# Performance work log

Hardware: AMD Instinct MI355X
Metric: run time of the kernel (lower is better)

The kernel has to match this reference:

```python
import jax, jax.numpy as jnp
import numpy as np

TEMPERATURE = 0.1
B, S, D, V = 4, 256, 768, 50257


def setup_inputs() -> dict:
    key = jax.random.key(0)
    k1, k2 = jax.random.split(key)
    return {
        "pred_embeds": jax.random.normal(k1, (B, S, D), dtype=jnp.float32),
        "embed_weight": jax.random.normal(k2, (V, D), dtype=jnp.float32),
    }


def reference(pred_embeds, embed_weight):
    # metric == 'l2': scores = -||p - t||^2, computed via the GEMM identity
    # -(||p||^2 + ||t||^2 - 2 p.t) instead of a (B,S,V,D) broadcast diff.
    p_sq = jnp.sum(pred_embeds * pred_embeds, axis=-1)        # (B,S)
    t_sq = jnp.sum(embed_weight * embed_weight, axis=-1)      # (V,)
    dot = jnp.einsum('bsd,vd->bsv', pred_embeds, embed_weight)  # (B,S,V)
    scores = 2.0 * dot - p_sq[..., None] - t_sq               # (B,S,V)

    softmax_pred_probs = jax.nn.softmax(scores / TEMPERATURE, axis=-1)
    predictions = jnp.argmax(softmax_pred_probs, axis=-1)      # (B,S) int

    # straight-through one-hot over probs
    y_hard = jax.nn.one_hot(predictions, V, dtype=softmax_pred_probs.dtype)
    pred_probs = y_hard - jax.lax.stop_gradient(softmax_pred_probs) + softmax_pred_probs

    # straight-through embedding lookup
    n_pred_embs = embed_weight[predictions]                    # (B,S,D)
    pred_embeds_st = pred_embeds + jax.lax.stop_gradient(n_pred_embs - pred_embeds)

    return (pred_embeds_st, pred_embeds, predictions, pred_probs, softmax_pred_probs)
```

## Files before the change

kernel.cpp:

```cpp
#include <hip/hip_runtime.h>
#include <math.h>

namespace {

constexpr int Bb = 4, Ss = 256, Dd = 768, Vv = 50257;
constexpr int Mm = Bb * Ss;
constexpr int BM = 128, BN = 128, BK = 32;
constexpr int NS = Dd / BK;
constexpr int TW = (Vv + BN - 1) / BN;
constexpr int TA = Mm / BM;
constexpr int NT2 = TW * 2;
constexpr int CHUNK = BM * BK;
constexpr float SC = 14.4269504088896341f;

constexpr int PSTRIDE = 17;
constexpr int PCOUNT  = 128 * 2 * PSTRIDE;
constexpr size_t SMEM_BYTES = (size_t)PCOUNT * 4 * 3;

typedef _Float16 f16x8 __attribute__((ext_vector_type(8)));
typedef float f32x4 __attribute__((ext_vector_type(4)));

constexpr size_t WPLANE = (size_t)TW * NS * CHUNK;
constexpr size_t APLANE = (size_t)TA * NS * CHUNK;

__device__ __forceinline__ void gload_lds16(const void* g, void* l) {
    typedef __attribute__((address_space(3))) void lds_t;
    typedef const __attribute__((address_space(1))) void gm_t;
    __builtin_amdgcn_global_load_lds((gm_t*)g, (lds_t*)l, 16, 0, 0);
}

__global__ __launch_bounds__(256) void convert_pack_tsq(const float* __restrict__ srcW,
                                                        const float* __restrict__ srcA,
                                                        _Float16* __restrict__ Whp,
                                                        _Float16* __restrict__ Wlp,
                                                        _Float16* __restrict__ Ahp,
                                                        _Float16* __restrict__ Alp,
                                                        float* __restrict__ tsq,
                                                        float* __restrict__ asq) {
    const bool isW = blockIdx.x < TW;
    const int t    = isW ? blockIdx.x : (blockIdx.x - TW);
    const int nrows = isW ? Vv : Mm;
    const float* __restrict__ src = isW ? srcW : srcA;
    _Float16* __restrict__ hp = isW ? Whp : Ahp;
    _Float16* __restrict__ lp = isW ? Wlp : Alp;
    float* __restrict__ sumsq = isW ? tsq : asq;

    const int tid = threadIdx.x;
    const int r   = blockIdx.y * 64 + (tid >> 2);
    const int q   = tid & 3;
    const int v   = t * BM + r;
    const bool valid = v < nrows;

    float sq = 0.f;
#pragma unroll
    for (int i = 0; i < 6; ++i) {
        const int s = q * 6 + i;
        float vals[32];
        if (valid) {
            const float4* p = reinterpret_cast<const float4*>(src + (size_t)v * Dd + s * BK);
#pragma unroll
            for (int k = 0; k < 8; ++k) *reinterpret_cast<float4*>(&vals[4 * k]) = p[k];
        } else {
#pragma unroll
            for (int k = 0; k < 32; ++k) vals[k] = 0.f;
        }
        const size_t chunk = ((size_t)t * NS + s) * CHUNK;
#pragma unroll
        for (int fq = 0; fq < 4; ++fq) {
            _Float16 hi8[8], lo8[8];
#pragma unroll
            for (int e = 0; e < 8; ++e) {
                const float x = vals[fq * 8 + e];
                sq = fmaf(x, x, sq);
                const _Float16 h = (_Float16)x;
                hi8[e] = h;
                lo8[e] = (_Float16)(x - (float)h);
            }
            *reinterpret_cast<f16x8*>(&hp[chunk + fq * (BM * 8) + (size_t)r * 8]) =
                *reinterpret_cast<const f16x8*>(hi8);
            *reinterpret_cast<f16x8*>(&lp[chunk + fq * (BM * 8) + (size_t)r * 8]) =
                *reinterpret_cast<const f16x8*>(lo8);
        }
    }
    sq += __shfl_xor(sq, 1);
    sq += __shfl_xor(sq, 2);
    if (valid && q == 0) sumsq[v] = sq;
}

__global__ __launch_bounds__(256) void gemm_kernel(const _Float16* __restrict__ Ahp,
                                                   const _Float16* __restrict__ Alp,
                                                   const _Float16* __restrict__ Whp,
                                                   const _Float16* __restrict__ Wlp,
                                                   const float* __restrict__ tsq,
                                                   float* __restrict__ scores,
                                                   float* __restrict__ pmax,
                                                   int*   __restrict__ pidx,
                                                   float* __restrict__ psum) {
    __shared__ __align__(16) char smem_raw[SMEM_BYTES];
    _Float16 (*lds)[CHUNK] = reinterpret_cast<_Float16(*)[CHUNK]>(smem_raw);

    const int b    = blockIdx.x;
    const int xcd  = b & 7;
    const int slot = b >> 3;
    const int tn   = xcd * 50 + (slot >> 3);
    const int tm   = slot & 7;
    if (tn >= TW) return;

    const int tid  = threadIdx.x;
    const int wid  = tid >> 6;
    const int lane = tid & 63;
    const int wr   = wid >> 1;
    const int wc   = wid & 1;
    const int fr   = lane & 15;
    const int fq   = lane >> 4;

    const _Float16* gA_h = Ahp + (size_t)tm * NS * CHUNK;
    const _Float16* gA_l = Alp + (size_t)tm * NS * CHUNK;
    const _Float16* gW_h = Whp + (size_t)tn * NS * CHUNK;
    const _Float16* gW_l = Wlp + (size_t)tn * NS * CHUNK;

    f32x4 acc[4][4];
#pragma unroll
    for (int m = 0; m < 4; ++m)
#pragma unroll
        for (int n = 0; n < 4; ++n) acc[m][n] = (f32x4){0.f, 0.f, 0.f, 0.f};

    for (int s = 0; s < NS; ++s) {
        if (s) __syncthreads();
        const size_t so = (size_t)s * CHUNK;
        const _Float16* gsrc[4] = {gA_h + so, gA_l + so, gW_h + so, gW_l + so};
#pragma unroll
        for (int c = 0; c < 4; ++c) {
#pragma unroll
            for (int i = 0; i < 2; ++i) {
                const int seg = wid * 2 + i;
                gload_lds16(gsrc[c] + seg * 512 + lane * 8, &lds[c][seg * 512]);
            }
        }
        __syncthreads();

        f16x8 ah[4], al[4];
#pragma unroll
        for (int m = 0; m < 4; ++m) {
            const int r = wr * 64 + m * 16 + fr;
            ah[m] = *reinterpret_cast<const f16x8*>(&lds[0][fq * (BM * 8) + r * 8]);
            al[m] = *reinterpret_cast<const f16x8*>(&lds[1][fq * (BM * 8) + r * 8]);
        }
#pragma unroll
        for (int n = 0; n < 4; ++n) {
            const int c = wc * 64 + n * 16 + fr;
            const f16x8 wh = *reinterpret_cast<const f16x8*>(&lds[2][fq * (BM * 8) + c * 8]);
            const f16x8 wl = *reinterpret_cast<const f16x8*>(&lds[3][fq * (BM * 8) + c * 8]);
#pragma unroll
            for (int m = 0; m < 4; ++m) {
                acc[m][n] = __builtin_amdgcn_mfma_f32_16x16x32_f16(ah[m], wh, acc[m][n], 0, 0, 0);
                acc[m][n] = __builtin_amdgcn_mfma_f32_16x16x32_f16(al[m], wh, acc[m][n], 0, 0, 0);
                acc[m][n] = __builtin_amdgcn_mfma_f32_16x16x32_f16(ah[m], wl, acc[m][n], 0, 0, 0);
            }
        }
    }

    __syncthreads();
    float* pmL = reinterpret_cast<float*>(smem_raw);
    float* psL = pmL + PCOUNT;
    int*   piL = reinterpret_cast<int*>(psL + PCOUNT);

    float tq[4];
    int   gcol[4];
    bool  ok[4];
#pragma unroll
    for (int n = 0; n < 4; ++n) {
        gcol[n] = tn * BN + wc * 64 + n * 16 + fr;
        ok[n]   = gcol[n] < Vv;
        tq[n]   = ok[n] ? tsq[gcol[n]] : 0.f;
    }

#pragma unroll
    for (int m = 0; m < 4; ++m) {
#pragma unroll
        for (int r = 0; r < 4; ++r) {
            const int rloc = wr * 64 + m * 16 + fq * 4 + r;
            const int grow = tm * BM + rloc;
            float vmax = -INFINITY;
            int   vidx = 0x7fffffff;
#pragma unroll
            for (int n = 0; n < 4; ++n) {
                if (ok[n]) {
                    const float sv = fmaf(2.f, acc[m][n][r], -tq[n]);
                    scores[(size_t)grow * Vv + gcol[n]] = sv;
                    if (sv > vmax) { vmax = sv; vidx = gcol[n]; }
                }
            }
            float ls = 0.f;
#pragma unroll
            for (int n = 0; n < 4; ++n) {
                if (ok[n]) {
                    const float sv = fmaf(2.f, acc[m][n][r], -tq[n]);
                    ls += exp2f((sv - vmax) * SC);
                }
            }
            const int o = (rloc * 2 + wc) * PSTRIDE + fr;
            pmL[o] = vmax;
            psL[o] = ls;
            piL[o] = vidx;
        }
    }
    __syncthreads();

    {
        const int rloc = tid >> 1;
        const int wcs  = tid & 1;
        float m = -INFINITY, s = 0.f;
        int   id = 0x7fffffff;
#pragma unroll
        for (int f = 0; f < 16; ++f) {
            const int o = (rloc * 2 + wcs) * PSTRIDE + f;
            const float m2 = pmL[o];
            const int   i2 = piL[o];
            const float s2 = psL[o];
            if (m2 > m || (m2 == m && i2 < id)) {
                s = ((m > -INFINITY) ? s * exp2f((m - m2) * SC) : 0.f) + s2;
                m = m2; id = i2;
            } else {
                s += s2 * exp2f((m2 - m) * SC);
            }
        }
        const int grow = tm * BM + rloc;
        const int cidx = tn * 2 + wcs;
        const size_t o = (size_t)grow * NT2 + cidx;
        pmax[o] = m;
        pidx[o] = id;
        psum[o] = s;
    }
}

__global__ __launch_bounds__(256) void reduce_stats(const float* __restrict__ pmax,
                                                    const int*   __restrict__ pidx,
                                                    const float* __restrict__ psum,
                                                    float* __restrict__ out1,
                                                    float* __restrict__ out2) {
    const int row = blockIdx.x;
    const int tid = threadIdx.x;
    const size_t base = (size_t)row * NT2;

    float m = -INFINITY, s = 0.f;
    int   id = 0x7fffffff;
    for (int c = tid; c < NT2; c += 256) {
        const float m2 = pmax[base + c];
        const int   i2 = pidx[base + c];
        const float s2 = psum[base + c];
        if (m2 > m || (m2 == m && i2 < id)) {
            s = ((m > -INFINITY) ? s * exp2f((m - m2) * SC) : 0.f) + s2;
            m = m2; id = i2;
        } else {
            s += (m2 > -INFINITY) ? s2 * exp2f((m2 - m) * SC) : 0.f;
        }
    }

    __shared__ float smax[256];
    __shared__ int   sidx[256];
    __shared__ float ssum[256];
    smax[tid] = m; sidx[tid] = id; ssum[tid] = s;
    __syncthreads();
#pragma unroll
    for (int off = 128; off > 0; off >>= 1) {
        if (tid < off) {
            const float m1 = smax[tid], m2 = smax[tid + off];
            const int   i1 = sidx[tid], i2 = sidx[tid + off];
            const float s1 = ssum[tid], s2 = ssum[tid + off];
            if (m2 > m1 || (m2 == m1 && i2 < i1)) {
                smax[tid] = m2; sidx[tid] = i2;
                ssum[tid] = ((m1 > -INFINITY) ? s1 * exp2f((m1 - m2) * SC) : 0.f) + s2;
            } else {
                ssum[tid] = s1 + ((m2 > -INFINITY) ? s2 * exp2f((m2 - m1) * SC) : 0.f);
            }
        }
        __syncthreads();
    }
    if (tid == 0) {
        out2[row] = (float)sidx[0];
        out1[(size_t)row * Dd + 766] = smax[0];
        out1[(size_t)row * Dd + 767] = 1.0f / ssum[0];
    }
}

__global__ __launch_bounds__(256) void finalize_kernel(const float* __restrict__ A,
                                                       const float* __restrict__ W,
                                                       float* __restrict__ out0,
                                                       float* __restrict__ out1,
                                                       float* __restrict__ out2,
                                                       float* __restrict__ out3,
                                                       float* __restrict__ out4) {
    const int row = blockIdx.x;
    const int tid = threadIdx.x;
    float* srow = out4 + (size_t)row * Vv;
    float* hrow = out3 + (size_t)row * Vv;
    constexpr int NV4 = Vv >> 2;

    const float gmax = out1[(size_t)row * Dd + 766];
    const float inv  = out1[(size_t)row * Dd + 767];
    const int   pred = (int)out2[row];

    const float4* s4 = reinterpret_cast<const float4*>(srow);
    float4* p4 = reinterpret_cast<float4*>(srow);
    float4* h4 = reinterpret_cast<float4*>(hrow);
    for (int i = tid; i < NV4; i += 256) {
        const float4 v = s4[i];
        const int b = 4 * i;
        float4 p, h;
        p.x = exp2f((v.x - gmax) * SC) * inv;
        p.y = exp2f((v.y - gmax) * SC) * inv;
        p.z = exp2f((v.z - gmax) * SC) * inv;
        p.w = exp2f((v.w - gmax) * SC) * inv;
        h.x = (b + 0 == pred) ? 1.f : 0.f;
        h.y = (b + 1 == pred) ? 1.f : 0.f;
        h.z = (b + 2 == pred) ? 1.f : 0.f;
        h.w = (b + 3 == pred) ? 1.f : 0.f;
        p4[i] = p;
        h4[i] = h;
    }
    if (tid == 0) {
        const float val = srow[Vv - 1];
        srow[Vv - 1] = exp2f((val - gmax) * SC) * inv;
        hrow[Vv - 1] = (pred == Vv - 1) ? 1.f : 0.f;
    }

    __syncthreads();

    const float4* wrow = reinterpret_cast<const float4*>(W + (size_t)pred * Dd);
    const float4* arow = reinterpret_cast<const float4*>(A + (size_t)row * Dd);
    float4* o0 = reinterpret_cast<float4*>(out0 + (size_t)row * Dd);
    float4* o1 = reinterpret_cast<float4*>(out1 + (size_t)row * Dd);
    if (tid < Dd / 4) {
        o0[tid] = wrow[tid];
        o1[tid] = arow[tid];
    }
}

}

extern "C" void kernel_launch(void* const* d_in, const int* in_sizes, int n_in,
                              void* d_out, int out_size, void* d_ws, size_t ws_size,
                              hipStream_t stream) {
    const float* pred_embeds  = (const float*)d_in[0];
    const float* embed_weight = (const float*)d_in[1];

    float* out  = (float*)d_out;
    float* out0 = out;
    float* out1 = out0 + (size_t)Mm * Dd;
    float* out2 = out1 + (size_t)Mm * Dd;
    float* out3 = out2 + Mm;
    float* out4 = out3 + (size_t)Mm * Vv;

    _Float16* Whp = (_Float16*)out3;
    _Float16* Wlp = Whp + WPLANE;
    _Float16* Ahp = Wlp + WPLANE;
    _Float16* Alp = Ahp + APLANE;
    float*    tsq = (float*)(Alp + APLANE);
    float*    asq = tsq + Vv;
    float*    pmax = asq + Mm;
    int*      pidx = (int*)(pmax + (size_t)Mm * NT2);
    float*    psum = (float*)(pidx + (size_t)Mm * NT2);

    convert_pack_tsq<<<dim3(TW + TA, 2), 256, 0, stream>>>(embed_weight, pred_embeds,
                                                           Whp, Wlp, Ahp, Alp, tsq, asq);

    gemm_kernel<<<3200, 256, 0, stream>>>(Ahp, Alp, Whp, Wlp, tsq, out4,
                                          pmax, pidx, psum);

    reduce_stats<<<Mm, 256, 0, stream>>>(pmax, pidx, psum, out1, out2);

    finalize_kernel<<<Mm, 256, 0, stream>>>(pred_embeds, embed_weight,
                                            out0, out1, out2, out3, out4);
}
```

Measured before the change: 490.0 us.

## Widen GEMM tile to 128x256 with 512 threads and fold reduce into finalize

The GEMM tile grows from 128x128 to 128x256 and runs with 8 waves per 512-thread block, so each A tile is reused across twice as many vocab columns. The tile-to-XCD mapping and the packed W layout are rebuilt to match. Row stats are now merged across lanes with shuffles inside the epilogue, and the separate reduce_stats kernel is removed, with its merge moved to the start of finalize_kernel. This cuts redundant A loads, one kernel launch and the epilogue LDS traffic, at the cost of more waves per block and fewer blocks, which may hurt occupancy or tail balance.

After: 654.0 us. 33.5% more time.

```diff
diff --git a/kernel.cpp b/kernel.cpp
--- a/kernel.cpp
+++ b/kernel.cpp
@@ -5,23 +5,24 @@
 
 constexpr int Bb = 4, Ss = 256, Dd = 768, Vv = 50257;
 constexpr int Mm = Bb * Ss;
-constexpr int BM = 128, BN = 128, BK = 32;
+constexpr int BM = 128, BN = 256, BK = 32;
 constexpr int NS = Dd / BK;
 constexpr int TW = (Vv + BN - 1) / BN;
 constexpr int TA = Mm / BM;
-constexpr int NT2 = TW * 2;
-constexpr int CHUNK = BM * BK;
+constexpr int NT4 = TW * 4;
+constexpr int CHA = BM * BK;
+constexpr int CHW = BN * BK;
 constexpr float SC = 14.4269504088896341f;
 
-constexpr int PSTRIDE = 17;
-constexpr int PCOUNT  = 128 * 2 * PSTRIDE;
-constexpr size_t SMEM_BYTES = (size_t)PCOUNT * 4 * 3;
+constexpr int PSTRIDE = 5;
+constexpr int PC = 128 * 4 * PSTRIDE;
+constexpr size_t SMEM_BYTES = 24576 * 2;
 
 typedef _Float16 f16x8 __attribute__((ext_vector_type(8)));
 typedef float f32x4 __attribute__((ext_vector_type(4)));
 
-constexpr size_t WPLANE = (size_t)TW * NS * CHUNK;
-constexpr size_t APLANE = (size_t)TA * NS * CHUNK;
+constexpr size_t WPLANE = (size_t)TW * NS * CHW;
+constexpr size_t APLANE = (size_t)TA * NS * CHA;
 
 __device__ __forceinline__ void gload_lds16(const void* g, void* l) {
     typedef __attribute__((address_space(3))) void lds_t;
@@ -37,18 +38,26 @@
                                                         _Float16* __restrict__ Alp,
                                                         float* __restrict__ tsq,
                                                         float* __restrict__ asq) {
-    const bool isW = blockIdx.x < TW;
-    const int t    = isW ? blockIdx.x : (blockIdx.x - TW);
-    const int nrows = isW ? Vv : Mm;
-    const float* __restrict__ src = isW ? srcW : srcA;
-    _Float16* __restrict__ hp = isW ? Whp : Ahp;
-    _Float16* __restrict__ lp = isW ? Wlp : Alp;
-    float* __restrict__ sumsq = isW ? tsq : asq;
+    const int gx  = blockIdx.x;
+    const bool isW = gx < TW * 4;
+    int t, rblk, nrows, tileRows, chunkE;
+    const float* __restrict__ src;
+    _Float16 *hp, *lp;
+    float* sumsq;
+    if (isW) {
+        t = gx >> 2; rblk = gx & 3; nrows = Vv; tileRows = 256; chunkE = CHW;
+        src = srcW; hp = Whp; lp = Wlp; sumsq = tsq;
+    } else {
+        const int u = gx - TW * 4;
+        t = u >> 1; rblk = u & 1; nrows = Mm; tileRows = 128; chunkE = CHA;
+        src = srcA; hp = Ahp; lp = Alp; sumsq = asq;
+    }
 
     const int tid = threadIdx.x;
-    const int r   = blockIdx.y * 64 + (tid >> 2);
+    const int r64 = tid >> 2;
     const int q   = tid & 3;
-    const int v   = t * BM + r;
+    const int rr  = rblk * 64 + r64;
+    const int v   = t * tileRows + rr;
     const bool valid = v < nrows;
 
     float sq = 0.f;
@@ -64,7 +73,7 @@
 #pragma unroll
             for (int k = 0; k < 32; ++k) vals[k] = 0.f;
         }
-        const size_t chunk = ((size_t)t * NS + s) * CHUNK;
+        const size_t chunk = ((size_t)t * NS + s) * chunkE;
 #pragma unroll
         for (int fq = 0; fq < 4; ++fq) {
             _Float16 hi8[8], lo8[8];
@@ -76,9 +85,9 @@
                 hi8[e] = h;
                 lo8[e] = (_Float16)(x - (float)h);
             }
-            *reinterpret_cast<f16x8*>(&hp[chunk + fq * (BM * 8) + (size_t)r * 8]) =
+            *reinterpret_cast<f16x8*>(&hp[chunk + fq * (tileRows * 8) + (size_t)rr * 8]) =
                 *reinterpret_cast<const f16x8*>(hi8);
-            *reinterpret_cast<f16x8*>(&lp[chunk + fq * (BM * 8) + (size_t)r * 8]) =
+            *reinterpret_cast<f16x8*>(&lp[chunk + fq * (tileRows * 8) + (size_t)rr * 8]) =
                 *reinterpret_cast<const f16x8*>(lo8);
         }
     }
@@ -87,7 +96,7 @@
     if (valid && q == 0) sumsq[v] = sq;
 }
 
-__global__ __launch_bounds__(256) void gemm_kernel(const _Float16* __restrict__ Ahp,
+__global__ __launch_bounds__(512) void gemm_kernel(const _Float16* __restrict__ Ahp,
                                                    const _Float16* __restrict__ Alp,
                                                    const _Float16* __restrict__ Whp,
                                                    const _Float16* __restrict__ Wlp,
@@ -97,27 +106,32 @@
                                                    int*   __restrict__ pidx,
                                                    float* __restrict__ psum) {
     __shared__ __align__(16) char smem_raw[SMEM_BYTES];
-    _Float16 (*lds)[CHUNK] = reinterpret_cast<_Float16(*)[CHUNK]>(smem_raw);
+    _Float16* ldsAh = reinterpret_cast<_Float16*>(smem_raw);
+    _Float16* ldsAl = ldsAh + CHA;
+    _Float16* ldsWh = ldsAl + CHA;
+    _Float16* ldsWl = ldsWh + CHW;
 
     const int b    = blockIdx.x;
     const int xcd  = b & 7;
     const int slot = b >> 3;
-    const int tn   = xcd * 50 + (slot >> 3);
+    const int ltn  = slot >> 3;
     const int tm   = slot & 7;
-    if (tn >= TW) return;
+    const int cnt  = (xcd < 5) ? 25 : 24;
+    if (ltn >= cnt) return;
+    const int tn   = ((xcd < 5) ? 25 * xcd : 125 + 24 * (xcd - 5)) + ltn;
 
     const int tid  = threadIdx.x;
     const int wid  = tid >> 6;
     const int lane = tid & 63;
-    const int wr   = wid >> 1;
-    const int wc   = wid & 1;
+    const int wr   = wid >> 2;
+    const int wc   = wid & 3;
     const int fr   = lane & 15;
     const int fq   = lane >> 4;
 
-    const _Float16* gA_h = Ahp + (size_t)tm * NS * CHUNK;
-    const _Float16* gA_l = Alp + (size_t)tm * NS * CHUNK;
-    const _Float16* gW_h = Whp + (size_t)tn * NS * CHUNK;
-    const _Float16* gW_l = Wlp + (size_t)tn * NS * CHUNK;
+    const _Float16* gA_h = Ahp + (size_t)tm * NS * CHA;
+    const _Float16* gA_l = Alp + (size_t)tm * NS * CHA;
+    const _Float16* gW_h = Whp + (size_t)tn * NS * CHW;
+    const _Float16* gW_l = Wlp + (size_t)tn * NS * CHW;
 
     f32x4 acc[4][4];
 #pragma unroll
@@ -127,15 +141,13 @@
 
     for (int s = 0; s < NS; ++s) {
         if (s) __syncthreads();
-        const size_t so = (size_t)s * CHUNK;
-        const _Float16* gsrc[4] = {gA_h + so, gA_l + so, gW_h + so, gW_l + so};
-#pragma unroll
-        for (int c = 0; c < 4; ++c) {
-#pragma unroll
-            for (int i = 0; i < 2; ++i) {
-                const int seg = wid * 2 + i;
-                gload_lds16(gsrc[c] + seg * 512 + lane * 8, &lds[c][seg * 512]);
-            }
+        gload_lds16(gA_h + (size_t)s * CHA + wid * 512 + lane * 8, ldsAh + wid * 512);
+        gload_lds16(gA_l + (size_t)s * CHA + wid * 512 + lane * 8, ldsAl + wid * 512);
+#pragma unroll
+        for (int i = 0; i < 2; ++i) {
+            const int seg = wid * 2 + i;
+            gload_lds16(gW_h + (size_t)s * CHW + seg * 512 + lane * 8, ldsWh + seg * 512);
+            gload_lds16(gW_l + (size_t)s * CHW + seg * 512 + lane * 8, ldsWl + seg * 512);
         }
         __syncthreads();
 
@@ -143,14 +155,14 @@
 #pragma unroll
         for (int m = 0; m < 4; ++m) {
             const int r = wr * 64 + m * 16 + fr;
-            ah[m] = *reinterpret_cast<const f16x8*>(&lds[0][fq * (BM * 8) + r * 8]);
-            al[m] = *reinterpret_cast<const f16x8*>(&lds[1][fq * (BM * 8) + r * 8]);
+            ah[m] = *reinterpret_cast<const f16x8*>(&ldsAh[fq * (BM * 8) + r * 8]);
+            al[m] = *reinterpret_cast<const f16x8*>(&ldsAl[fq * (BM * 8) + r * 8]);
         }
 #pragma unroll
         for (int n = 0; n < 4; ++n) {
             const int c = wc * 64 + n * 16 + fr;
-            const f16x8 wh = *reinterpret_cast<const f16x8*>(&lds[2][fq * (BM * 8) + c * 8]);
-            const f16x8 wl = *reinterpret_cast<const f16x8*>(&lds[3][fq * (BM * 8) + c * 8]);
+            const f16x8 wh = *reinterpret_cast<const f16x8*>(&ldsWh[fq * (BN * 8) + c * 8]);
+            const f16x8 wl = *reinterpret_cast<const f16x8*>(&ldsWl[fq * (BN * 8) + c * 8]);
 #pragma unroll
             for (int m = 0; m < 4; ++m) {
                 acc[m][n] = __builtin_amdgcn_mfma_f32_16x16x32_f16(ah[m], wh, acc[m][n], 0, 0, 0);
@@ -162,8 +174,8 @@
 
     __syncthreads();
     float* pmL = reinterpret_cast<float*>(smem_raw);
-    float* psL = pmL + PCOUNT;
-    int*   piL = reinterpret_cast<int*>(psL + PCOUNT);
+    float* psL = pmL + PC;
+    int*   piL = reinterpret_cast<int*>(psL + PC);
 
     float tq[4];
     int   gcol[4];
@@ -181,111 +193,77 @@
         for (int r = 0; r < 4; ++r) {
             const int rloc = wr * 64 + m * 16 + fq * 4 + r;
             const int grow = tm * BM + rloc;
+            float sv[4];
             float vmax = -INFINITY;
             int   vidx = 0x7fffffff;
 #pragma unroll
             for (int n = 0; n < 4; ++n) {
+                sv[n] = ok[n] ? fmaf(2.f, acc[m][n][r], -tq[n]) : -INFINITY;
                 if (ok[n]) {
-                    const float sv = fmaf(2.f, acc[m][n][r], -tq[n]);
-                    scores[(size_t)grow * Vv + gcol[n]] = sv;
-                    if (sv > vmax) { vmax = sv; vidx = gcol[n]; }
+                    scores[(size_t)grow * Vv + gcol[n]] = sv[n];
+                    if (sv[n] > vmax) { vmax = sv[n]; vidx = gcol[n]; }
                 }
             }
             float ls = 0.f;
-#pragma unroll
-            for (int n = 0; n < 4; ++n) {
-                if (ok[n]) {
-                    const float sv = fmaf(2.f, acc[m][n][r], -tq[n]);
-                    ls += exp2f((sv - vmax) * SC);
+            if (vmax > -INFINITY) {
+#pragma unroll
+                for (int n = 0; n < 4; ++n)
+                    if (ok[n]) ls += exp2f((sv[n] - vmax) * SC);
+            }
+#pragma unroll
+            for (int off = 1; off <= 2; off <<= 1) {
+                const float om = __shfl_xor(vmax, off);
+                const int   oi = __shfl_xor(vidx, off);
+                const float os = __shfl_xor(ls,  off);
+                if (om > vmax || (om == vmax && om > -INFINITY && oi < vidx)) {
+                    ls = ((vmax > -INFINITY) ? ls * exp2f((vmax - om) * SC) : 0.f) + os;
+                    vmax = om; vidx = oi;
+                } else if (om > -INFINITY) {
+                    ls += os * exp2f((om - vmax) * SC);
                 }
             }
-            const int o = (rloc * 2 + wc) * PSTRIDE + fr;
-            pmL[o] = vmax;
-            psL[o] = ls;
-            piL[o] = vidx;
+            if ((fr & 3) == 0) {
+                const int o = (rloc * 4 + wc) * PSTRIDE + (fr >> 2);
+                pmL[o] = vmax;
+                psL[o] = ls;
+                piL[o] = vidx;
+            }
         }
     }
     __syncthreads();
 
     {
-        const int rloc = tid >> 1;
-        const int wcs  = tid & 1;
+        const int rloc = tid >> 2;
+        const int wcs  = tid & 3;
         float m = -INFINITY, s = 0.f;
         int   id = 0x7fffffff;
 #pragma unroll
-        for (int f = 0; f < 16; ++f) {
-            const int o = (rloc * 2 + wcs) * PSTRIDE + f;
+        for (int f = 0; f < 4; ++f) {
+            const int o = (rloc * 4 + wcs) * PSTRIDE + f;
             const float m2 = pmL[o];
             const int   i2 = piL[o];
             const float s2 = psL[o];
-            if (m2 > m || (m2 == m && i2 < id)) {
+            if (m2 > m || (m2 == m && m2 > -INFINITY && i2 < id)) {
                 s = ((m > -INFINITY) ? s * exp2f((m - m2) * SC) : 0.f) + s2;
                 m = m2; id = i2;
-            } else {
+            } else if (m2 > -INFINITY) {
                 s += s2 * exp2f((m2 - m) * SC);
             }
         }
         const int grow = tm * BM + rloc;
-        const int cidx = tn * 2 + wcs;
-        const size_t o = (size_t)grow * NT2 + cidx;
+        const int cidx = tn * 4 + wcs;
+        const size_t o = (size_t)grow * NT4 + cidx;
         pmax[o] = m;
         pidx[o] = id;
         psum[o] = s;
     }
 }
 
-__global__ __launch_bounds__(256) void reduce_stats(const float* __restrict__ pmax,
-                                                    const int*   __restrict__ pidx,
-                                                    const float* __restrict__ psum,
-                                                    float* __restrict__ out1,
-                                                    float* __restrict__ out2) {
-    const int row = blockIdx.x;
-    const int tid = threadIdx.x;
-    const size_t base = (size_t)row * NT2;
-
-    float m = -INFINITY, s = 0.f;
-    int   id = 0x7fffffff;
-    for (int c = tid; c < NT2; c += 256) {
-        const float m2 = pmax[base + c];
-        const int   i2 = pidx[base + c];
-        const float s2 = psum[base + c];
-        if (m2 > m || (m2 == m && i2 < id)) {
-            s = ((m > -INFINITY) ? s * exp2f((m - m2) * SC) : 0.f) + s2;
-            m = m2; id = i2;
-        } else {
-            s += (m2 > -INFINITY) ? s2 * exp2f((m2 - m) * SC) : 0.f;
-        }
-    }
-
-    __shared__ float smax[256];
-    __shared__ int   sidx[256];
-    __shared__ float ssum[256];
-    smax[tid] = m; sidx[tid] = id; ssum[tid] = s;
-    __syncthreads();
-#pragma unroll
-    for (int off = 128; off > 0; off >>= 1) {
-        if (tid < off) {
-            const float m1 = smax[tid], m2 = smax[tid + off];
-            const int   i1 = sidx[tid], i2 = sidx[tid + off];
-            const float s1 = ssum[tid], s2 = ssum[tid + off];
-            if (m2 > m1 || (m2 == m1 && i2 < i1)) {
-                smax[tid] = m2; sidx[tid] = i2;
-                ssum[tid] = ((m1 > -INFINITY) ? s1 * exp2f((m1 - m2) * SC) : 0.f) + s2;
-            } else {
-                ssum[tid] = s1 + ((m2 > -INFINITY) ? s2 * exp2f((m2 - m1) * SC) : 0.f);
-            }
-        }
-        __syncthreads();
-    }
-    if (tid == 0) {
-        out2[row] = (float)sidx[0];
-        out1[(size_t)row * Dd + 766] = smax[0];
-        out1[(size_t)row * Dd + 767] = 1.0f / ssum[0];
-    }
-}
-
 __global__ __launch_bounds__(256) void finalize_kernel(const float* __restrict__ A,
                                                        const float* __restrict__ W,
+                                                       const float* __restrict__ pmax,
+                                                       const int*   __restrict__ pidx,
+                                                       const float* __restrict__ psum,
                                                        float* __restrict__ out0,
                                                        float* __restrict__ out1,
                                                        float* __restrict__ out2,
@@ -297,9 +275,44 @@
     float* hrow = out3 + (size_t)row * Vv;
     constexpr int NV4 = Vv >> 2;
 
-    const float gmax = out1[(size_t)row * Dd + 766];
-    const float inv  = out1[(size_t)row * Dd + 767];
-    const int   pred = (int)out2[row];
+    const size_t base = (size_t)row * NT4;
+    float m = -INFINITY, s = 0.f;
+    int   id = 0x7fffffff;
+    for (int c = tid; c < NT4; c += 256) {
+        const float m2 = pmax[base + c];
+        const int   i2 = pidx[base + c];
+        const float s2 = psum[base + c];
+        if (m2 > m || (m2 == m && m2 > -INFINITY && i2 < id)) {
+            s = ((m > -INFINITY) ? s * exp2f((m - m2) * SC) : 0.f) + s2;
+            m = m2; id = i2;
+        } else if (m2 > -INFINITY) {
+            s += s2 * exp2f((m2 - m) * SC);
+        }
+    }
+    __shared__ float smax[256];
+    __shared__ int   sidx[256];
+    __shared__ float ssum[256];
+    smax[tid] = m; sidx[tid] = id; ssum[tid] = s;
+    __syncthreads();
+#pragma unroll
+    for (int off = 128; off > 0; off >>= 1) {
+        if (tid < off) {
+            const float m1 = smax[tid], m2 = smax[tid + off];
+            const int   i1 = sidx[tid], i2 = sidx[tid + off];
+            const float s1 = ssum[tid], s2 = ssum[tid + off];
+            if (m2 > m1 || (m2 == m1 && m2 > -INFINITY && i2 < i1)) {
+                smax[tid] = m2; sidx[tid] = i2;
+                ssum[tid] = ((m1 > -INFINITY) ? s1 * exp2f((m1 - m2) * SC) : 0.f) + s2;
+            } else if (m2 > -INFINITY) {
+                ssum[tid] = s1 + s2 * exp2f((m2 - m1) * SC);
+            }
+        }
+        __syncthreads();
+    }
+    const float gmax = smax[0];
+    const int   pred = sidx[0];
+    const float inv  = 1.0f / ssum[0];
+    __syncthreads();
 
     const float4* s4 = reinterpret_cast<const float4*>(srow);
     float4* p4 = reinterpret_cast<float4*>(srow);
@@ -323,9 +336,8 @@
         const float val = srow[Vv - 1];
         srow[Vv - 1] = exp2f((val - gmax) * SC) * inv;
         hrow[Vv - 1] = (pred == Vv - 1) ? 1.f : 0.f;
-    }
-
-    __syncthreads();
+        out2[row] = (float)pred;
+    }
 
     const float4* wrow = reinterpret_cast<const float4*>(W + (size_t)pred * Dd);
     const float4* arow = reinterpret_cast<const float4*>(A + (size_t)row * Dd);
@@ -359,17 +371,16 @@
     float*    tsq = (float*)(Alp + APLANE);
     float*    asq = tsq + Vv;
     float*    pmax = asq + Mm;
-    int*      pidx = (int*)(pmax + (size_t)Mm * NT2);
-    float*    psum = (float*)(pidx + (size_t)Mm * NT2);
-
-    convert_pack_tsq<<<dim3(TW + TA, 2), 256, 0, stream>>>(embed_weight, pred_embeds,
-                                                           Whp, Wlp, Ahp, Alp, tsq, asq);
-
-    gemm_kernel<<<3200, 256, 0, stream>>>(Ahp, Alp, Whp, Wlp, tsq, out4,
+    int*      pidx = (int*)(pmax + (size_t)Mm * NT4);
+    float*    psum = (float*)(pidx + (size_t)Mm * NT4);
+
+    convert_pack_tsq<<<TW * 4 + TA * 2, 256, 0, stream>>>(embed_weight, pred_embeds,
+                                                          Whp, Wlp, Ahp, Alp, tsq, asq);
+
+    gemm_kernel<<<1600, 512, 0, stream>>>(Ahp, Alp, Whp, Wlp, tsq, out4,
                                           pmax, pidx, psum);
 
-    reduce_stats<<<Mm, 256, 0, stream>>>(pmax, pidx, psum, out1, out2);
-
     finalize_kernel<<<Mm, 256, 0, stream>>>(pred_embeds, embed_weight,
+                                            pmax, pidx, psum,
                                             out0, out1, out2, out3, out4);
 }
```
